# Optimization experiments

Measured on AMD Instinct MI355X. Metric: run time of the kernel, lower is better.

## Reference

```python
import jax, jax.numpy as jnp
import numpy as np
import math

D_MODEL = 1024
MEM_SIZE = 4096
N_HEADS = 8
BATCH = 4
SEQ = 1024
TOP_K = min(SEQ, MEM_SIZE // 10)  # 409, matches torch: min(seq_len, memory_size//10)
UPDATE_RATE = 0.01


def _gelu(x):
    return jax.nn.gelu(x, approximate=False)  # torch nn.GELU default (erf)


def setup_inputs() -> dict:
    key = jax.random.key(0)
    ks = jax.random.split(key, 26)
    w = lambda k, shape, s=0.02: (jax.random.normal(k, shape, jnp.float32) * s)
    inp = {
        "x": jax.random.normal(ks[0], (BATCH, SEQ, D_MODEL), jnp.float32),
        "memory_bank": jax.random.normal(ks[1], (MEM_SIZE, D_MODEL), jnp.float32) * 0.1,
        "memory_indices": jax.random.randint(ks[2], (BATCH, TOP_K), 0, MEM_SIZE, jnp.int32),
        # memory_encoder: Linear -> GELU -> Linear
        "enc_w1": w(ks[3], (D_MODEL, D_MODEL)), "enc_b1": jnp.zeros((D_MODEL,), jnp.float32),
        "enc_w2": w(ks[4], (D_MODEL, D_MODEL)), "enc_b2": jnp.zeros((D_MODEL,), jnp.float32),
        # MultiheadAttention in/out projections
        "wq": w(ks[5], (D_MODEL, D_MODEL)), "bq": jnp.zeros((D_MODEL,), jnp.float32),
        "wk": w(ks[6], (D_MODEL, D_MODEL)), "bk": jnp.zeros((D_MODEL,), jnp.float32),
        "wv": w(ks[7], (D_MODEL, D_MODEL)), "bv": jnp.zeros((D_MODEL,), jnp.float32),
        "wo": w(ks[8], (D_MODEL, D_MODEL)), "bo": jnp.zeros((D_MODEL,), jnp.float32),
        # memory_decoder: Linear -> GELU -> Linear
        "dec_w1": w(ks[9], (D_MODEL, D_MODEL)), "dec_b1": jnp.zeros((D_MODEL,), jnp.float32),
        "dec_w2": w(ks[10], (D_MODEL, D_MODEL)), "dec_b2": jnp.zeros((D_MODEL,), jnp.float32),
        # LayerNorm
        "ln_g": jnp.ones((D_MODEL,), jnp.float32), "ln_b": jnp.zeros((D_MODEL,), jnp.float32),
        # importance_scorer: Linear(d,64) -> GELU -> Linear(64,1) -> Sigmoid
        "imp_w1": w(ks[11], (D_MODEL, 64)), "imp_b1": jnp.zeros((64,), jnp.float32),
        "imp_w2": w(ks[12], (64, 1)), "imp_b2": jnp.zeros((1,), jnp.float32),
    }
    return inp


def reference(x, memory_bank, memory_indices,
              enc_w1, enc_b1, enc_w2, enc_b2,
              wq, bq, wk, bk, wv, bv, wo, bo,
              dec_w1, dec_b1, dec_w2, dec_b2,
              ln_g, ln_b, imp_w1, imp_b1, imp_w2, imp_b2):
    B, L, D = x.shape
    M = memory_bank.shape[0]
    H = N_HEADS
    dh = D // H

    # memory_encoder (dropout inactive at eval)
    enc = _gelu(x @ enc_w1 + enc_b1) @ enc_w2 + enc_b2  # [B,L,D]

    # cross-attention: query = encoded input, key/value = memory bank (shared across batch)
    q = (enc @ wq + bq).reshape(B, L, H, dh)
    k = (memory_bank @ wk + bk).reshape(M, H, dh)
    v = (memory_bank @ wv + bv).reshape(M, H, dh)
    scores = jnp.einsum('blhd,mhd->bhlm', q, k) * (1.0 / math.sqrt(dh))
    attn = jax.nn.softmax(scores, axis=-1)                 # [B,H,L,M]
    ctx = jnp.einsum('bhlm,mhd->blhd', attn, v).reshape(B, L, D)
    mem_out = ctx @ wo + bo

    # memory_decoder + residual + LayerNorm
    dec = _gelu(mem_out @ dec_w1 + dec_b1) @ dec_w2 + dec_b2
    comb = x + dec
    mu = jnp.mean(comb, axis=-1, keepdims=True)
    var = jnp.var(comb, axis=-1, keepdims=True)
    out = (comb - mu) / jnp.sqrt(var + 1e-5) * ln_g + ln_b  # [B,L,D]

    # _update_memory: importance top-k select + sequential EMA scatter into memory bank
    imp = jax.nn.sigmoid(_gelu(x @ imp_w1 + imp_b1) @ imp_w2 + imp_b2)[..., 0]  # [B,L]
    _, top_idx = jax.lax.top_k(imp, TOP_K)                  # [B,K]
    top_tok = jnp.take_along_axis(x, top_idx[..., None], axis=1)  # [B,K,D]

    # faithful to the torch double loop (b outer, k inner): sequential EMA with
    # chained updates on index collisions
    flat_idx = memory_indices.reshape(-1)
    flat_tok = top_tok.reshape(-1, D)

    def body(mem, xs):
        i, t = xs
        row = (1.0 - UPDATE_RATE) * mem[i] + UPDATE_RATE * t
        return mem.at[i].set(row), None

    new_mem, _ = jax.lax.scan(body, memory_bank, (flat_idx, flat_tok))
    return out, new_mem
```

## Files before the change

### kernel.cpp

```cpp
#include <hip/hip_runtime.h>

typedef unsigned short u16;
typedef __attribute__((ext_vector_type(4))) int i4;
typedef __attribute__((ext_vector_type(4))) unsigned u4;
typedef __attribute__((ext_vector_type(4))) unsigned short us4;
typedef __attribute__((ext_vector_type(8))) short short8;
typedef __attribute__((ext_vector_type(4))) float f4;

#define D_MODEL 1024
#define ROWS 4096
#define NHEAD 8
#define DH 128
#define TOPK 409
#define NUPD 1636
#define NBATCH 4
#define MAXC 64
#define ATTNROWS 32768

__device__ __forceinline__ u16 f2bf(float f) {
  unsigned u = __builtin_bit_cast(unsigned, f);
  u += 0x7fffu + ((u >> 16) & 1u);
  return (u16)(u >> 16);
}
__device__ __forceinline__ float bf2f(u16 b) {
  unsigned u = ((unsigned)b) << 16;
  return __builtin_bit_cast(float, u);
}
__device__ __forceinline__ float gelu_f(float v) {
  return 0.5f * v * (1.0f + erff(v * 0.70710678118654752f));
}
__device__ __forceinline__ void gload16(const void* g, void* l) {
  __builtin_amdgcn_global_load_lds((const __attribute__((address_space(1))) void*)g,
                                   (__attribute__((address_space(3))) void*)l, 16, 0, 0);
}

__global__ __launch_bounds__(256) void conv_kernel(const float* __restrict__ in,
                                                   u16* __restrict__ out, int n4) {
  int i = blockIdx.x * 256 + threadIdx.x;
  if (i < n4) {
    f4 v = ((const f4*)in)[i];
    us4 o;
    o.x = f2bf(v.x); o.y = f2bf(v.y); o.z = f2bf(v.z); o.w = f2bf(v.w);
    ((us4*)out)[i] = o;
  }
}

__global__ __launch_bounds__(256) void wtrans8_kernel(const float* s0, const float* s1,
                                                      const float* s2, const float* s3,
                                                      const float* s4, const float* s5,
                                                      const float* s6, const float* s7,
                                                      u16* __restrict__ dst) {
  const float* srcs[8] = {s0, s1, s2, s3, s4, s5, s6, s7};
  const float* w = srcs[blockIdx.z];
  u16* wt = dst + (size_t)blockIdx.z * (1024 * 1024);
  __shared__ float t[32][33];
  int tx = threadIdx.x & 31, ty = threadIdx.x >> 5;
  int k0 = blockIdx.y * 32, n0 = blockIdx.x * 32;
  for (int r = 0; r < 4; ++r)
    t[ty + r * 8][tx] = w[(size_t)(k0 + ty + r * 8) * 1024 + n0 + tx];
  __syncthreads();
  for (int r = 0; r < 4; ++r)
    wt[(size_t)(n0 + ty + r * 8) * 1024 + k0 + tx] = f2bf(t[tx][ty + r * 8]);
}

template <int EPI>
__global__ __launch_bounds__(256) void gemm_bt(const u16* __restrict__ A,
                                               const u16* __restrict__ BT,
                                               const float* __restrict__ bias,
                                               void* __restrict__ C) {
  __shared__ __align__(16) char al[2 * 128 * 64];
  __shared__ __align__(16) char bl[2 * 64 * 64];
  const int K = 1024, N = 1024;
  const int id = blockIdx.x;
  const int xcd = id & 7, j = id >> 3;
  const int m0 = ((j & 3) * 8 + xcd) * 128;
  const int n0 = (j >> 2) * 64;
  const int tid = threadIdx.x;
  const int lane = tid & 63, wid = tid >> 6;
  const int g = lane >> 4, qi = lane & 15;
  const int wr = wid >> 1, wc = wid & 1;
  f4 acc[4][2] = {};

  const int a0r = tid >> 2, a0b = (tid & 3) ^ ((a0r >> 1) & 3);
  const int c1 = tid + 256;
  const int a1r = c1 >> 2, a1b = (c1 & 3) ^ ((a1r >> 1) & 3);
  const int b0r = tid >> 2, b0b = (tid & 3) ^ ((b0r >> 1) & 3);

#define STAGE(buf, kt)                                                                   \
  {                                                                                      \
    const int k0_ = (kt) * 32;                                                           \
    gload16(A + (size_t)(m0 + a0r) * K + k0_ + a0b * 8, al + (buf) * 8192 + tid * 16);   \
    gload16(A + (size_t)(m0 + a1r) * K + k0_ + a1b * 8, al + (buf) * 8192 + c1 * 16);    \
    gload16(BT + (size_t)(n0 + b0r) * K + k0_ + b0b * 8, bl + (buf) * 4096 + tid * 16);  \
  }

  STAGE(0, 0);
  __syncthreads();
  int cur = 0;
  for (int kt = 0; kt < 32; ++kt) {
    if (kt + 1 < 32) STAGE(cur ^ 1, kt + 1);
    short8 af[4], bfr[2];
    for (int i = 0; i < 4; ++i) {
      int r = wr * 64 + i * 16 + qi;
      af[i] = *(const short8*)(al + cur * 8192 + r * 64 + ((g ^ ((r >> 1) & 3))) * 16);
    }
    for (int sn = 0; sn < 2; ++sn) {
      int r = wc * 32 + sn * 16 + qi;
      bfr[sn] = *(const short8*)(bl + cur * 4096 + r * 64 + ((g ^ ((r >> 1) & 3))) * 16);
    }
    for (int i = 0; i < 4; ++i)
      for (int sn = 0; sn < 2; ++sn)
        acc[i][sn] = __builtin_amdgcn_mfma_f32_16x16x32_bf16(af[i], bfr[sn], acc[i][sn], 0, 0, 0);
    __syncthreads();
    cur ^= 1;
  }
#undef STAGE

  for (int i = 0; i < 4; ++i) {
    int row = m0 + wr * 64 + i * 16 + g * 4;
    for (int sn = 0; sn < 2; ++sn) {
      int col = n0 + wc * 32 + sn * 16 + qi;
      float bv = bias[col];
      for (int jj = 0; jj < 4; ++jj) {
        float v = acc[i][sn][jj] + bv;
        if constexpr (EPI == 1) v = gelu_f(v);
        if constexpr (EPI == 2)
          ((float*)C)[(size_t)(row + jj) * N + col] = v;
        else
          ((u16*)C)[(size_t)(row + jj) * N + col] = f2bf(v);
      }
    }
  }
}

__global__ __launch_bounds__(256) void gemm_kv(const u16* __restrict__ A,
                                               const u16* __restrict__ BT,
                                               const float* __restrict__ bk,
                                               const float* __restrict__ bv,
                                               u16* __restrict__ Ck, u16* __restrict__ CvT) {
  __shared__ __align__(16) char pool[2 * 128 * 64 + 2 * 64 * 64];
  char* al = pool;
  char* bl = pool + 2 * 128 * 64;
  const int id = blockIdx.x;
  const int xcd = id & 7, j = id >> 3;
  const int m0 = ((j & 3) * 8 + xcd) * 128;
  const int n0 = (j >> 2) * 64;
  const int tid = threadIdx.x;
  const int lane = tid & 63, wid = tid >> 6;
  const int g = lane >> 4, qi = lane & 15;
  const int wr = wid >> 1, wc = wid & 1;
  const int K = 1024, M = 4096;
  f4 acc[4][2] = {};

  const int a0r = tid >> 2, a0b = (tid & 3) ^ ((a0r >> 1) & 3);
  const int c1 = tid + 256;
  const int a1r = c1 >> 2, a1b = (c1 & 3) ^ ((a1r >> 1) & 3);
  const int b0r = tid >> 2, b0b = (tid & 3) ^ ((b0r >> 1) & 3);

#define STAGE(buf, kt)                                                                   \
  {                                                                                      \
    const int k0_ = (kt) * 32;                                                           \
    gload16(A + (size_t)(m0 + a0r) * K + k0_ + a0b * 8, al + (buf) * 8192 + tid * 16);   \
    gload16(A + (size_t)(m0 + a1r) * K + k0_ + a1b * 8, al + (buf) * 8192 + c1 * 16);    \
    gload16(BT + (size_t)(n0 + b0r) * K + k0_ + b0b * 8, bl + (buf) * 4096 + tid * 16);  \
  }

  STAGE(0, 0);
  __syncthreads();
  int cur = 0;
  for (int kt = 0; kt < 32; ++kt) {
    if (kt + 1 < 32) STAGE(cur ^ 1, kt + 1);
    short8 af[4], bfr[2];
    for (int i = 0; i < 4; ++i) {
      int r = wr * 64 + i * 16 + qi;
      af[i] = *(const short8*)(al + cur * 8192 + r * 64 + ((g ^ ((r >> 1) & 3))) * 16);
    }
    for (int sn = 0; sn < 2; ++sn) {
      int r = wc * 32 + sn * 16 + qi;
      bfr[sn] = *(const short8*)(bl + cur * 4096 + r * 64 + ((g ^ ((r >> 1) & 3))) * 16);
    }
    for (int i = 0; i < 4; ++i)
      for (int sn = 0; sn < 2; ++sn)
        acc[i][sn] = __builtin_amdgcn_mfma_f32_16x16x32_bf16(af[i], bfr[sn], acc[i][sn], 0, 0, 0);
    __syncthreads();
    cur ^= 1;
  }
#undef STAGE

  if (n0 < 1024) {
    for (int i = 0; i < 4; ++i) {
      int row = m0 + wr * 64 + i * 16 + g * 4;
      for (int sn = 0; sn < 2; ++sn) {
        int col = n0 + wc * 32 + sn * 16 + qi;
        float bvv = bk[col];
        for (int jj = 0; jj < 4; ++jj)
          Ck[(size_t)(row + jj) * 1024 + col] = f2bf(acc[i][sn][jj] + bvv);
      }
    }
  } else {
    u16(*t)[132] = (u16(*)[132])pool;
    __syncthreads();
    for (int i = 0; i < 4; ++i)
      for (int sn = 0; sn < 2; ++sn) {
        int nl = wc * 32 + sn * 16 + qi;
        float bvv = bv[n0 - 1024 + nl];
        for (int jj = 0; jj < 4; ++jj)
          t[nl][wr * 64 + i * 16 + g * 4 + jj] = f2bf(acc[i][sn][jj] + bvv);
      }
    __syncthreads();
    int r = tid >> 2, cg = tid & 3;
    for (int v = 0; v < 4; ++v) {
      us4 val = *(const us4*)&t[r][cg * 32 + v * 8];
      *(us4*)&CvT[(size_t)(n0 - 1024 + r) * M + m0 + cg * 32 + v * 8] = val;
    }
  }
}

template <int LP>
__global__ __launch_bounds__(512) void attn_kernel(const u16* __restrict__ q,
                                                   const u16* __restrict__ kp,
                                                   const u16* __restrict__ vT,
                                                   u16* __restrict__ cp0, u16* __restrict__ cp1,
                                                   u16* __restrict__ cp2, u16* __restrict__ cp3,
                                                   float* __restrict__ ml) {
  constexpr int MR = 4096 >> LP;
  constexpr int NT = MR / 64;
  __shared__ __align__(16) char kl[64 * 256];
  __shared__ __align__(16) char vl[128 * 128];
  const int id = blockIdx.x;
  const int h = id & 7;
  const int rest = id >> 3;
  const int part = rest & ((1 << LP) - 1);
  const int qblk = (rest >> LP) & 7;
  const int b = rest >> (3 + LP);
  const int tid = threadIdx.x;
  const int lane = tid & 63, wid = tid >> 6;
  const int g = lane >> 4, qi = lane & 15;
  const int qrow = b * 1024 + qblk * 128 + wid * 16 + qi;
  const float scale = 0.08838834764831845f;
  u16* ctp = (part == 0) ? cp0 : (part == 1) ? cp1 : (part == 2) ? cp2 : cp3;

  short8 qf[4];
  for (int kk = 0; kk < 4; ++kk)
    qf[kk] = *(const short8*)(q + (size_t)qrow * 1024 + h * 128 + kk * 32 + g * 8);

  const int kc0 = tid, kc1 = tid + 512;
  const int kr0 = kc0 >> 4, kb0 = kc0 & 15, kr1 = kc1 >> 4, kb1 = kc1 & 15;
  const int vr0 = kc0 >> 3, vb0 = kc0 & 7, vr1 = kc1 >> 3, vb1 = kc1 & 7;
  const int kd0 = kr0 * 256 + (kb0 ^ (kr0 & 7)) * 16;
  const int kd1 = kr1 * 256 + (kb1 ^ (kr1 & 7)) * 16;
  const int vd0 = vr0 * 128 + (vb0 ^ (vr0 & 7)) * 16;
  const int vd1 = vr1 * 128 + (vb1 ^ (vr1 & 7)) * 16;
  const int mbase = part * MR;
  const u16* kg0 = kp + (size_t)kr0 * 1024 + h * 128 + kb0 * 8;
  const u16* kg1 = kp + (size_t)kr1 * 1024 + h * 128 + kb1 * 8;
  const u16* vg0 = vT + (size_t)(h * 128 + vr0) * 4096 + vb0 * 8;
  const u16* vg1 = vT + (size_t)(h * 128 + vr1) * 4096 + vb1 * 8;

  i4 kreg0, kreg1, vreg0, vreg1;
#define LOADREGS(mt_)                                  \
  {                                                    \
    const int m0_ = mbase + (mt_) * 64;                \
    kreg0 = *(const i4*)(kg0 + (size_t)m0_ * 1024);    \
    kreg1 = *(const i4*)(kg1 + (size_t)m0_ * 1024);    \
    vreg0 = *(const i4*)(vg0 + m0_);                   \
    vreg1 = *(const i4*)(vg1 + m0_);                   \
  }

  f4 ct[8] = {};
  float mrun = -1e30f, lsum = 0.0f;

  LOADREGS(0);
  for (int mt = 0; mt < NT; ++mt) {
    __syncthreads();
    *(i4*)(kl + kd0) = kreg0;
    *(i4*)(kl + kd1) = kreg1;
    *(i4*)(vl + vd0) = vreg0;
    *(i4*)(vl + vd1) = vreg1;
    __syncthreads();
    if (mt + 1 < NT) LOADREGS(mt + 1);

    f4 st[4] = {};
    for (int s = 0; s < 4; ++s) {
      int n = s * 16 + qi;
      const char* krow = kl + n * 256;
      int sw = n & 7;
      for (int kk = 0; kk < 4; ++kk) {
        short8 a = *(const short8*)(krow + ((kk * 4 + g) ^ sw) * 16);
        st[s] = __builtin_amdgcn_mfma_f32_16x16x32_bf16(a, qf[kk], st[s], 0, 0, 0);
      }
    }
    float sv[16];
    float tmax = -1e30f;
    for (int s = 0; s < 4; ++s)
      for (int jj = 0; jj < 4; ++jj) {
        float v = st[s][jj] * scale;
        sv[s * 4 + jj] = v;
        tmax = fmaxf(tmax, v);
      }
    tmax = fmaxf(tmax, __shfl_xor(tmax, 16, 64));
    tmax = fmaxf(tmax, __shfl_xor(tmax, 32, 64));
    float mnew = fmaxf(mrun, tmax);
    float r = __expf(mrun - mnew);
    float psum = 0.0f;
    for (int i = 0; i < 16; ++i) {
      sv[i] = __expf(sv[i] - mnew);
      psum += sv[i];
    }
    psum += __shfl_xor(psum, 16, 64);
    psum += __shfl_xor(psum, 32, 64);
    lsum = lsum * r + psum;
    mrun = mnew;
    for (int i = 0; i < 8; ++i) ct[i] = ct[i] * r;

    unsigned pk0[4], pk1[4];
    for (int s = 0; s < 4; ++s) {
      pk0[s] = (unsigned)f2bf(sv[s * 4 + 0]) | ((unsigned)f2bf(sv[s * 4 + 1]) << 16);
      pk1[s] = (unsigned)f2bf(sv[s * 4 + 2]) | ((unsigned)f2bf(sv[s * 4 + 3]) << 16);
    }
    const int src1 = qi + ((g & 1) << 5);
    const int src2 = src1 + 16;
    const bool hi = (g & 2) != 0;
    for (int p = 0; p < 2; ++p) {
      unsigned a0 = __shfl(pk0[2 * p], src1, 64), b0 = __shfl(pk0[2 * p + 1], src1, 64);
      unsigned a1 = __shfl(pk1[2 * p], src1, 64), b1 = __shfl(pk1[2 * p + 1], src1, 64);
      unsigned a2 = __shfl(pk0[2 * p], src2, 64), b2 = __shfl(pk0[2 * p + 1], src2, 64);
      unsigned a3 = __shfl(pk1[2 * p], src2, 64), b3 = __shfl(pk1[2 * p + 1], src2, 64);
      u4 bw;
      bw.x = hi ? b0 : a0; bw.y = hi ? b1 : a1; bw.z = hi ? b2 : a2; bw.w = hi ? b3 : a3;
      short8 pf = __builtin_bit_cast(short8, bw);
      for (int d = 0; d < 8; ++d) {
        int dr = d * 16 + qi;
        short8 a = *(const short8*)(vl + dr * 128 + (((p * 4 + g) ^ (dr & 7))) * 16);
        ct[d] = __builtin_amdgcn_mfma_f32_16x16x32_bf16(a, pf, ct[d], 0, 0, 0);
      }
    }
  }
#undef LOADREGS

  const int orow = ((b * 8 + h) << 10) + qblk * 128 + wid * 16 + qi;
  if (g == 0) {
    ml[(size_t)(part * ATTNROWS + orow) * 2 + 0] = mrun;
    ml[(size_t)(part * ATTNROWS + orow) * 2 + 1] = lsum;
  }
  for (int d = 0; d < 8; ++d) {
    us4 o;
    o.x = f2bf(ct[d][0]); o.y = f2bf(ct[d][1]);
    o.z = f2bf(ct[d][2]); o.w = f2bf(ct[d][3]);
    *(us4*)(ctp + (size_t)orow * 128 + d * 16 + g * 4) = o;
  }
}

__global__ __launch_bounds__(256) void combine4_kernel(const u16* __restrict__ cp0,
                                                       const u16* __restrict__ cp1,
                                                       const u16* __restrict__ cp2,
                                                       const u16* __restrict__ cp3,
                                                       const float* __restrict__ ml,
                                                       u16* __restrict__ ctx) {
  int tid = threadIdx.x;
  int row = blockIdx.x * 16 + (tid >> 4);
  int dp = (tid & 15) * 8;
  float m0 = ml[(size_t)row * 2], l0 = ml[(size_t)row * 2 + 1];
  float m1 = ml[((size_t)ATTNROWS + row) * 2], l1 = ml[((size_t)ATTNROWS + row) * 2 + 1];
  float m2 = ml[((size_t)2 * ATTNROWS + row) * 2], l2 = ml[((size_t)2 * ATTNROWS + row) * 2 + 1];
  float m3 = ml[((size_t)3 * ATTNROWS + row) * 2], l3 = ml[((size_t)3 * ATTNROWS + row) * 2 + 1];
  float m = fmaxf(fmaxf(m0, m1), fmaxf(m2, m3));
  float s0 = __expf(m0 - m), s1 = __expf(m1 - m), s2 = __expf(m2 - m), s3 = __expf(m3 - m);
  float inv = 1.0f / (l0 * s0 + l1 * s1 + l2 * s2 + l3 * s3);
  short8 c0 = *(const short8*)(cp0 + (size_t)row * 128 + dp);
  short8 c1 = *(const short8*)(cp1 + (size_t)row * 128 + dp);
  short8 c2 = *(const short8*)(cp2 + (size_t)row * 128 + dp);
  short8 c3 = *(const short8*)(cp3 + (size_t)row * 128 + dp);
  us4 o[2];
  for (int i = 0; i < 8; ++i) {
    float f = (bf2f((u16)c0[i]) * s0 + bf2f((u16)c1[i]) * s1 + bf2f((u16)c2[i]) * s2 +
               bf2f((u16)c3[i]) * s3) * inv;
    ((u16*)o)[i] = f2bf(f);
  }
  int bb = row >> 13, hh = (row >> 10) & 7, qr = row & 1023;
  *(short8*)(ctx + (size_t)((bb << 10) + qr) * 1024 + hh * 128 + dp) =
      __builtin_bit_cast(short8, o);
}

__global__ __launch_bounds__(256) void ln_kernel(const float* __restrict__ x,
                                                 const float* __restrict__ dec,
                                                 const float* __restrict__ gw,
                                                 const float* __restrict__ bw,
                                                 float* __restrict__ out,
                                                 int* __restrict__ cnt) {
  __shared__ float rs[256], rs2[256];
  int row = blockIdx.x, tid = threadIdx.x;
  if (tid == 0) cnt[row] = 0;
  float c[4];
  float s = 0.0f, s2 = 0.0f;
  for (int i = 0; i < 4; ++i) {
    int col = tid + i * 256;
    float v = x[(size_t)row * 1024 + col] + dec[(size_t)row * 1024 + col];
    c[i] = v; s += v; s2 += v * v;
  }
  rs[tid] = s; rs2[tid] = s2;
  __syncthreads();
  for (int st = 128; st > 0; st >>= 1) {
    if (tid < st) { rs[tid] += rs[tid + st]; rs2[tid] += rs2[tid + st]; }
    __syncthreads();
  }
  float mu = rs[0] * (1.0f / 1024.0f);
  float var = rs2[0] * (1.0f / 1024.0f) - mu * mu;
  float inv = rsqrtf(var + 1e-5f);
  for (int i = 0; i < 4; ++i) {
    int col = tid + i * 256;
    out[(size_t)row * 1024 + col] = (c[i] - mu) * inv * gw[col] + bw[col];
  }
}

__global__ __launch_bounds__(256) void imp_kernel(const float* __restrict__ x,
                                                  const float* __restrict__ w1,
                                                  const float* __restrict__ b1,
                                                  const float* __restrict__ w2,
                                                  const float* __restrict__ b2,
                                                  float* __restrict__ imp) {
  __shared__ float xs[8][1024];
  int tid = threadIdx.x;
  int lane = tid & 63, wid = tid >> 6;
  size_t base = (size_t)blockIdx.x * 8192;
  for (int i = 0; i < 32; ++i) ((float*)xs)[tid + i * 256] = x[base + tid + i * 256];
  __syncthreads();
  int r0 = wid * 2, r1 = wid * 2 + 1;
  float a0 = 0.0f, a1 = 0.0f;
  for (int k = 0; k < 1024; ++k) {
    float wv = w1[k * 64 + lane];
    a0 += xs[r0][k] * wv;
    a1 += xs[r1][k] * wv;
  }
  float h0 = gelu_f(a0 + b1[lane]) * w2[lane];
  float h1 = gelu_f(a1 + b1[lane]) * w2[lane];
  for (int d = 1; d < 64; d <<= 1) {
    h0 += __shfl_xor(h0, d, 64);
    h1 += __shfl_xor(h1, d, 64);
  }
  if (lane == 0) {
    imp[blockIdx.x * 8 + r0] = 1.0f / (1.0f + expf(-(h0 + b2[0])));
    imp[blockIdx.x * 8 + r1] = 1.0f / (1.0f + expf(-(h1 + b2[0])));
  }
}

__global__ __launch_bounds__(512) void topk_kernel(const float* __restrict__ imp,
                                                   int* __restrict__ tidx) {
  __shared__ float v[1024];
  __shared__ int ix[1024];
  int b = blockIdx.x, tid = threadIdx.x;
  for (int i = tid; i < 1024; i += 512) { v[i] = imp[b * 1024 + i]; ix[i] = i; }
  __syncthreads();
  for (int k = 2; k <= 1024; k <<= 1) {
    for (int j = k >> 1; j > 0; j >>= 1) {
      for (int t = tid; t < 1024; t += 512) {
        int p = t ^ j;
        if (p > t) {
          float va = v[t], vb = v[p];
          int ia = ix[t], ib = ix[p];
          bool ord = (va > vb) || (va == vb && ia < ib);
          bool up = ((t & k) == 0);
          if (up ? !ord : ord) { v[t] = vb; v[p] = va; ix[t] = ib; ix[p] = ia; }
        }
      }
      __syncthreads();
    }
  }
  for (int t = tid; t < TOPK; t += 512) tidx[b * TOPK + t] = ix[t];
}

__global__ __launch_bounds__(128) void rank_kernel(const int* __restrict__ midx,
                                                   int* __restrict__ cnt,
                                                   int* __restrict__ slot) {
  __shared__ int mi[NUPD];
  int tid = threadIdx.x;
  for (int i = tid; i < NUPD; i += 128) mi[i] = midx[i];
  __syncthreads();
  int j = blockIdx.x * 128 + tid;
  if (j < NUPD) {
    int r = mi[j], rank = 0;
    for (int jp = 0; jp < j; ++jp) rank += (mi[jp] == r) ? 1 : 0;
    if (rank < MAXC) slot[r * MAXC + rank] = j;
    atomicAdd(&cnt[r], 1);
  }
}

__global__ __launch_bounds__(256) void apply_kernel(const float* __restrict__ x,
                                                    const float* __restrict__ mem,
                                                    const int* __restrict__ tidx,
                                                    const int* __restrict__ cnt,
                                                    const int* __restrict__ slot,
                                                    float* __restrict__ outm) {
  int row = blockIdx.x, tid = threadIdx.x;
  f4 acc = ((const f4*)(mem + (size_t)row * 1024))[tid];
  int c = cnt[row];
  c = c < MAXC ? c : MAXC;
  for (int t = 0; t < c; ++t) {
    int j = slot[row * MAXC + t];
    int b = j / TOPK;
    int tr = tidx[j];
    f4 xv = ((const f4*)(x + ((size_t)b * 1024 + tr) * 1024))[tid];
    acc = acc * 0.99f + xv * 0.01f;
  }
  ((f4*)(outm + (size_t)row * 1024))[tid] = acc;
}

extern "C" void kernel_launch(void* const* d_in, const int* in_sizes, int n_in,
                              void* d_out, int out_size, void* d_ws, size_t ws_size,
                              hipStream_t stream) {
  const float* x = (const float*)d_in[0];
  const float* memory_bank = (const float*)d_in[1];
  const int* memory_indices = (const int*)d_in[2];
  const float* enc_w1 = (const float*)d_in[3];
  const float* enc_b1 = (const float*)d_in[4];
  const float* enc_w2 = (const float*)d_in[5];
  const float* enc_b2 = (const float*)d_in[6];
  const float* wq = (const float*)d_in[7];
  const float* bq = (const float*)d_in[8];
  const float* wk = (const float*)d_in[9];
  const float* bk = (const float*)d_in[10];
  const float* wv = (const float*)d_in[11];
  const float* bv = (const float*)d_in[12];
  const float* wo = (const float*)d_in[13];
  const float* bo = (const float*)d_in[14];
  const float* dec_w1 = (const float*)d_in[15];
  const float* dec_b1 = (const float*)d_in[16];
  const float* dec_w2 = (const float*)d_in[17];
  const float* dec_b2 = (const float*)d_in[18];
  const float* ln_g = (const float*)d_in[19];
  const float* ln_b = (const float*)d_in[20];
  const float* imp_w1 = (const float*)d_in[21];
  const float* imp_b1 = (const float*)d_in[22];
  const float* imp_w2 = (const float*)d_in[23];
  const float* imp_b2 = (const float*)d_in[24];

  char* ws = (char*)d_ws;
  u16* buf0 = (u16*)(ws);
  u16* buf1 = (u16*)(ws + (8ull << 20));
  u16* buf2 = (u16*)(ws + (16ull << 20));
  u16* buf3 = (u16*)(ws + (24ull << 20));
  u16* buf4 = (u16*)(ws + (32ull << 20));
  float* decb = (float*)(ws + (40ull << 20));
  u16* wtb = (u16*)(ws + (56ull << 20));
  float* impb = (float*)(ws + (72ull << 20));
  int* tidx = (int*)(ws + (72ull << 20) + (1 << 16));
  int* cnt = (int*)buf3;
  int* slot = (int*)(ws + (24ull << 20) + (1 << 16));
  u16* cp0 = buf0;
  u16* cp1 = buf2;
  u16* cp2 = (u16*)(ws + (40ull << 20));
  u16* cp3 = (u16*)(ws + (48ull << 20));
  float* ml = (float*)(ws + (56ull << 20));

  const int NM = 1024 * 1024;
  u16* wt_e1 = wtb + 0 * NM;
  u16* wt_e2 = wtb + 1 * NM;
  u16* wt_q = wtb + 2 * NM;
  u16* wt_k = wtb + 3 * NM;
  u16* wt_o = wtb + 5 * NM;
  u16* wt_d1 = wtb + 6 * NM;
  u16* wt_d2 = wtb + 7 * NM;

  conv_kernel<<<4096, 256, 0, stream>>>(x, buf0, ROWS * D_MODEL / 4);
  conv_kernel<<<4096, 256, 0, stream>>>(memory_bank, buf2, ROWS * D_MODEL / 4);
  wtrans8_kernel<<<dim3(32, 32, 8), 256, 0, stream>>>(enc_w1, enc_w2, wq, wk, wv, wo,
                                                      dec_w1, dec_w2, wtb);

  gemm_bt<1><<<512, 256, 0, stream>>>(buf0, wt_e1, enc_b1, buf1);
  gemm_bt<0><<<512, 256, 0, stream>>>(buf1, wt_e2, enc_b2, buf0);
  gemm_bt<0><<<512, 256, 0, stream>>>(buf0, wt_q, bq, buf1);
  gemm_kv<<<1024, 256, 0, stream>>>(buf2, wt_k, bk, bv, buf3, buf4);

  attn_kernel<2><<<1024, 512, 0, stream>>>(buf1, buf3, buf4, cp0, cp1, cp2, cp3, ml);
  combine4_kernel<<<2048, 256, 0, stream>>>(cp0, cp1, cp2, cp3, ml, buf1);

  gemm_bt<0><<<512, 256, 0, stream>>>(buf1, wt_o, bo, buf0);
  gemm_bt<1><<<512, 256, 0, stream>>>(buf0, wt_d1, dec_b1, buf2);
  gemm_bt<2><<<512, 256, 0, stream>>>(buf2, wt_d2, dec_b2, decb);
  ln_kernel<<<4096, 256, 0, stream>>>(x, decb, ln_g, ln_b, (float*)d_out, cnt);

  imp_kernel<<<512, 256, 0, stream>>>(x, imp_w1, imp_b1, imp_w2, imp_b2, impb);
  topk_kernel<<<NBATCH, 512, 0, stream>>>(impb, tidx);
  rank_kernel<<<13, 128, 0, stream>>>(memory_indices, cnt, slot);
  apply_kernel<<<4096, 256, 0, stream>>>(x, memory_bank, tidx, cnt, slot,
                                         (float*)d_out + (size_t)ROWS * D_MODEL);
}
```

Measured before the change: 442.2 us.

## Fold back-to-back linear layers into precomputed weight products and merge GEMM launches

Enc_w2 and wq are multiplied into one combined weight, and likewise wo and dec_w1, because no nonlinearity sits between them. The weight-product GEMMs and their folded biases run inside one mega kernel together with the KV projection and the first encoder GEMM. This removes two full activation GEMMs and several launches from the critical path, and the two input conversions become a single launch. The cost is extra weight-weight GEMMs on every call and rounding of the combined weights to bf16, which may change numerical error.

```diff
diff --git a/kernel.cpp b/kernel.cpp
--- a/kernel.cpp
+++ b/kernel.cpp
@@ -34,15 +34,18 @@
                                    (__attribute__((address_space(3))) void*)l, 16, 0, 0);
 }
 
-__global__ __launch_bounds__(256) void conv_kernel(const float* __restrict__ in,
-                                                   u16* __restrict__ out, int n4) {
-  int i = blockIdx.x * 256 + threadIdx.x;
-  if (i < n4) {
-    f4 v = ((const f4*)in)[i];
-    us4 o;
-    o.x = f2bf(v.x); o.y = f2bf(v.y); o.z = f2bf(v.z); o.w = f2bf(v.w);
-    ((us4*)out)[i] = o;
-  }
+__global__ __launch_bounds__(256) void conv2_kernel(const float* __restrict__ in0,
+                                                    u16* __restrict__ out0,
+                                                    const float* __restrict__ in1,
+                                                    u16* __restrict__ out1, int nb) {
+  int bid = blockIdx.x;
+  const float* in = (bid < nb) ? in0 : in1;
+  u16* out = (bid < nb) ? out0 : out1;
+  int i = (bid < nb ? bid : bid - nb) * 256 + threadIdx.x;
+  f4 v = ((const f4*)in)[i];
+  us4 o;
+  o.x = f2bf(v.x); o.y = f2bf(v.y); o.z = f2bf(v.z); o.w = f2bf(v.w);
+  ((us4*)out)[i] = o;
 }
 
 __global__ __launch_bounds__(256) void wtrans8_kernel(const float* s0, const float* s1,
@@ -63,6 +66,166 @@
     wt[(size_t)(n0 + ty + r * 8) * 1024 + k0 + tx] = f2bf(t[tx][ty + r * 8]);
 }
 
+__global__ __launch_bounds__(256) void bias_partB(const float* __restrict__ pbuf,
+                                                  const float* __restrict__ bq,
+                                                  const float* __restrict__ db1,
+                                                  float* __restrict__ bqp,
+                                                  float* __restrict__ bodp) {
+  int id = blockIdx.x;
+  int which = id >> 2;
+  int n = (id & 3) * 256 + threadIdx.x;
+  float s = 0.0f;
+  for (int kb = 0; kb < 8; ++kb) s += pbuf[(size_t)(which * 8 + kb) * 1024 + n];
+  float* out = which ? bodp : bqp;
+  const float* badd = which ? db1 : bq;
+  out[n] = s + badd[n];
+}
+
+__device__ __forceinline__ void gemm_core(const u16* __restrict__ A,
+                                          const u16* __restrict__ BT,
+                                          char* al, char* bl, int m0, int n0,
+                                          f4 acc[4][2]) {
+  const int K = 1024;
+  const int tid = threadIdx.x;
+  const int lane = tid & 63;
+  const int g = lane >> 4, qi = lane & 15;
+  const int wid = tid >> 6;
+  const int wr = wid >> 1, wc = wid & 1;
+  const int a0r = tid >> 2, a0b = (tid & 3) ^ ((a0r >> 1) & 3);
+  const int c1 = tid + 256;
+  const int a1r = c1 >> 2, a1b = (c1 & 3) ^ ((a1r >> 1) & 3);
+  const int b0r = tid >> 2, b0b = (tid & 3) ^ ((b0r >> 1) & 3);
+
+#define STAGE(buf, kt)                                                                   \
+  {                                                                                      \
+    const int k0_ = (kt) * 32;                                                           \
+    gload16(A + (size_t)(m0 + a0r) * K + k0_ + a0b * 8, al + (buf) * 8192 + tid * 16);   \
+    gload16(A + (size_t)(m0 + a1r) * K + k0_ + a1b * 8, al + (buf) * 8192 + c1 * 16);    \
+    gload16(BT + (size_t)(n0 + b0r) * K + k0_ + b0b * 8, bl + (buf) * 4096 + tid * 16);  \
+  }
+
+  STAGE(0, 0);
+  __syncthreads();
+  int cur = 0;
+  for (int kt = 0; kt < 32; ++kt) {
+    if (kt + 1 < 32) STAGE(cur ^ 1, kt + 1);
+    short8 af[4], bfr[2];
+    for (int i = 0; i < 4; ++i) {
+      int r = wr * 64 + i * 16 + qi;
+      af[i] = *(const short8*)(al + cur * 8192 + r * 64 + ((g ^ ((r >> 1) & 3))) * 16);
+    }
+    for (int sn = 0; sn < 2; ++sn) {
+      int r = wc * 32 + sn * 16 + qi;
+      bfr[sn] = *(const short8*)(bl + cur * 4096 + r * 64 + ((g ^ ((r >> 1) & 3))) * 16);
+    }
+    for (int i = 0; i < 4; ++i)
+      for (int sn = 0; sn < 2; ++sn)
+        acc[i][sn] = __builtin_amdgcn_mfma_f32_16x16x32_bf16(af[i], bfr[sn], acc[i][sn], 0, 0, 0);
+    __syncthreads();
+    cur ^= 1;
+  }
+#undef STAGE
+}
+
+__global__ __launch_bounds__(256) void mega_kernel(
+    const u16* __restrict__ Akv, const u16* __restrict__ BTkv,
+    const float* __restrict__ bk, const float* __restrict__ bv,
+    u16* __restrict__ Ck, u16* __restrict__ CvT,
+    const u16* __restrict__ Ae, const u16* __restrict__ BTe,
+    const float* __restrict__ be, u16* __restrict__ Ce,
+    const u16* __restrict__ A0, const u16* __restrict__ B0, u16* __restrict__ C0,
+    const u16* __restrict__ A1, const u16* __restrict__ B1, u16* __restrict__ C1,
+    const float* __restrict__ b2, const float* __restrict__ wqf,
+    const float* __restrict__ bo, const float* __restrict__ dw1,
+    float* __restrict__ pbuf) {
+  __shared__ __align__(16) char pool[2 * 128 * 64 + 2 * 64 * 64];
+  char* al = pool;
+  char* bl = pool + 2 * 128 * 64;
+  const int gid = blockIdx.x;
+  const int tid = threadIdx.x;
+  const int lane = tid & 63, wid = tid >> 6;
+  const int g = lane >> 4, qi = lane & 15;
+  const int wr = wid >> 1, wc = wid & 1;
+
+  if (gid < 1024) {
+    const int xcd = gid & 7, j = gid >> 3;
+    const int m0 = ((j & 3) * 8 + xcd) * 128;
+    const int n0 = (j >> 2) * 64;
+    f4 acc[4][2] = {};
+    gemm_core(Akv, BTkv, al, bl, m0, n0, acc);
+    if (n0 < 1024) {
+      for (int i = 0; i < 4; ++i) {
+        int row = m0 + wr * 64 + i * 16 + g * 4;
+        for (int sn = 0; sn < 2; ++sn) {
+          int col = n0 + wc * 32 + sn * 16 + qi;
+          float bvv = bk[col];
+          for (int jj = 0; jj < 4; ++jj)
+            Ck[(size_t)(row + jj) * 1024 + col] = f2bf(acc[i][sn][jj] + bvv);
+        }
+      }
+    } else {
+      u16(*t)[132] = (u16(*)[132])pool;
+      __syncthreads();
+      for (int i = 0; i < 4; ++i)
+        for (int sn = 0; sn < 2; ++sn) {
+          int nl = wc * 32 + sn * 16 + qi;
+          float bvv = bv[n0 - 1024 + nl];
+          for (int jj = 0; jj < 4; ++jj)
+            t[nl][wr * 64 + i * 16 + g * 4 + jj] = f2bf(acc[i][sn][jj] + bvv);
+        }
+      __syncthreads();
+      int r = tid >> 2, cg = tid & 3;
+      for (int v = 0; v < 4; ++v) {
+        us4 val = *(const us4*)&t[r][cg * 32 + v * 8];
+        *(us4*)&CvT[(size_t)(n0 - 1024 + r) * 4096 + m0 + cg * 32 + v * 8] = val;
+      }
+    }
+  } else if (gid < 1536) {
+    const int id = gid - 1024;
+    const int xcd = id & 7, j = id >> 3;
+    const int m0 = ((j & 3) * 8 + xcd) * 128;
+    const int n0 = (j >> 2) * 64;
+    f4 acc[4][2] = {};
+    gemm_core(Ae, BTe, al, bl, m0, n0, acc);
+    for (int i = 0; i < 4; ++i) {
+      int row = m0 + wr * 64 + i * 16 + g * 4;
+      for (int sn = 0; sn < 2; ++sn) {
+        int col = n0 + wc * 32 + sn * 16 + qi;
+        float bv = be[col];
+        for (int jj = 0; jj < 4; ++jj)
+          Ce[(size_t)(row + jj) * 1024 + col] = f2bf(gelu_f(acc[i][sn][jj] + bv));
+      }
+    }
+  } else if (gid < 1792) {
+    const int id = gid - 1536;
+    const int which = id >> 7, j = id & 127;
+    const u16* A = which ? A1 : A0;
+    const u16* BT = which ? B1 : B0;
+    u16* C = which ? C1 : C0;
+    const int m0 = (j >> 4) * 128, n0 = (j & 15) * 64;
+    f4 acc[4][2] = {};
+    gemm_core(A, BT, al, bl, m0, n0, acc);
+    for (int i = 0; i < 4; ++i) {
+      int row = m0 + wr * 64 + i * 16 + g * 4;
+      for (int sn = 0; sn < 2; ++sn) {
+        int col = n0 + wc * 32 + sn * 16 + qi;
+        for (int jj = 0; jj < 4; ++jj)
+          C[(size_t)(row + jj) * 1024 + col] = f2bf(acc[i][sn][jj]);
+      }
+    }
+  } else {
+    const int lid = gid - 1792;
+    const int which = lid >> 5;
+    const int kb = (lid >> 2) & 7;
+    const int n = (lid & 3) * 256 + tid;
+    const float* bvec = which ? bo : b2;
+    const float* W = which ? dw1 : wqf;
+    float s = 0.0f;
+    for (int k = kb * 128; k < kb * 128 + 128; ++k) s += bvec[k] * W[(size_t)k * 1024 + n];
+    pbuf[(size_t)(which * 8 + kb) * 1024 + n] = s;
+  }
+}
+
 template <int EPI>
 __global__ __launch_bounds__(256) void gemm_bt(const u16* __restrict__ A,
                                                const u16* __restrict__ BT,
@@ -70,7 +233,7 @@
                                                void* __restrict__ C) {
   __shared__ __align__(16) char al[2 * 128 * 64];
   __shared__ __align__(16) char bl[2 * 64 * 64];
-  const int K = 1024, N = 1024;
+  const int N = 1024;
   const int id = blockIdx.x;
   const int xcd = id & 7, j = id >> 3;
   const int m0 = ((j & 3) * 8 + xcd) * 128;
@@ -80,42 +243,7 @@
   const int g = lane >> 4, qi = lane & 15;
   const int wr = wid >> 1, wc = wid & 1;
   f4 acc[4][2] = {};
-
-  const int a0r = tid >> 2, a0b = (tid & 3) ^ ((a0r >> 1) & 3);
-  const int c1 = tid + 256;
-  const int a1r = c1 >> 2, a1b = (c1 & 3) ^ ((a1r >> 1) & 3);
-  const int b0r = tid >> 2, b0b = (tid & 3) ^ ((b0r >> 1) & 3);
-
-#define STAGE(buf, kt)                                                                   \
-  {                                                                                      \
-    const int k0_ = (kt) * 32;                                                           \
-    gload16(A + (size_t)(m0 + a0r) * K + k0_ + a0b * 8, al + (buf) * 8192 + tid * 16);   \
-    gload16(A + (size_t)(m0 + a1r) * K + k0_ + a1b * 8, al + (buf) * 8192 + c1 * 16);    \
-    gload16(BT + (size_t)(n0 + b0r) * K + k0_ + b0b * 8, bl + (buf) * 4096 + tid * 16);  \
-  }
-
-  STAGE(0, 0);
-  __syncthreads();
-  int cur = 0;
-  for (int kt = 0; kt < 32; ++kt) {
-    if (kt + 1 < 32) STAGE(cur ^ 1, kt + 1);
-    short8 af[4], bfr[2];
-    for (int i = 0; i < 4; ++i) {
-      int r = wr * 64 + i * 16 + qi;
-      af[i] = *(const short8*)(al + cur * 8192 + r * 64 + ((g ^ ((r >> 1) & 3))) * 16);
-    }
-    for (int sn = 0; sn < 2; ++sn) {
-      int r = wc * 32 + sn * 16 + qi;
-      bfr[sn] = *(const short8*)(bl + cur * 4096 + r * 64 + ((g ^ ((r >> 1) & 3))) * 16);
-    }
-    for (int i = 0; i < 4; ++i)
-      for (int sn = 0; sn < 2; ++sn)
-        acc[i][sn] = __builtin_amdgcn_mfma_f32_16x16x32_bf16(af[i], bfr[sn], acc[i][sn], 0, 0, 0);
-    __syncthreads();
-    cur ^= 1;
-  }
-#undef STAGE
-
+  gemm_core(A, BT, al, bl, m0, n0, acc);
   for (int i = 0; i < 4; ++i) {
     int row = m0 + wr * 64 + i * 16 + g * 4;
     for (int sn = 0; sn < 2; ++sn) {
@@ -129,89 +257,6 @@
         else
           ((u16*)C)[(size_t)(row + jj) * N + col] = f2bf(v);
       }
-    }
-  }
-}
-
-__global__ __launch_bounds__(256) void gemm_kv(const u16* __restrict__ A,
-                                               const u16* __restrict__ BT,
-                                               const float* __restrict__ bk,
-                                               const float* __restrict__ bv,
-                                               u16* __restrict__ Ck, u16* __restrict__ CvT) {
-  __shared__ __align__(16) char pool[2 * 128 * 64 + 2 * 64 * 64];
-  char* al = pool;
-  char* bl = pool + 2 * 128 * 64;
-  const int id = blockIdx.x;
-  const int xcd = id & 7, j = id >> 3;
-  const int m0 = ((j & 3) * 8 + xcd) * 128;
-  const int n0 = (j >> 2) * 64;
-  const int tid = threadIdx.x;
-  const int lane = tid & 63, wid = tid >> 6;
-  const int g = lane >> 4, qi = lane & 15;
-  const int wr = wid >> 1, wc = wid & 1;
-  const int K = 1024, M = 4096;
-  f4 acc[4][2] = {};
-
-  const int a0r = tid >> 2, a0b = (tid & 3) ^ ((a0r >> 1) & 3);
-  const int c1 = tid + 256;
-  const int a1r = c1 >> 2, a1b = (c1 & 3) ^ ((a1r >> 1) & 3);
-  const int b0r = tid >> 2, b0b = (tid & 3) ^ ((b0r >> 1) & 3);
-
-#define STAGE(buf, kt)                                                                   \
-  {                                                                                      \
-    const int k0_ = (kt) * 32;                                                           \
-    gload16(A + (size_t)(m0 + a0r) * K + k0_ + a0b * 8, al + (buf) * 8192 + tid * 16);   \
-    gload16(A + (size_t)(m0 + a1r) * K + k0_ + a1b * 8, al + (buf) * 8192 + c1 * 16);    \
-    gload16(BT + (size_t)(n0 + b0r) * K + k0_ + b0b * 8, bl + (buf) * 4096 + tid * 16);  \
-  }
-
-  STAGE(0, 0);
-  __syncthreads();
-  int cur = 0;
-  for (int kt = 0; kt < 32; ++kt) {
-    if (kt + 1 < 32) STAGE(cur ^ 1, kt + 1);
-    short8 af[4], bfr[2];
-    for (int i = 0; i < 4; ++i) {
-      int r = wr * 64 + i * 16 + qi;
-      af[i] = *(const short8*)(al + cur * 8192 + r * 64 + ((g ^ ((r >> 1) & 3))) * 16);
-    }
-    for (int sn = 0; sn < 2; ++sn) {
-      int r = wc * 32 + sn * 16 + qi;
-      bfr[sn] = *(const short8*)(bl + cur * 4096 + r * 64 + ((g ^ ((r >> 1) & 3))) * 16);
-    }
-    for (int i = 0; i < 4; ++i)
-      for (int sn = 0; sn < 2; ++sn)
-        acc[i][sn] = __builtin_amdgcn_mfma_f32_16x16x32_bf16(af[i], bfr[sn], acc[i][sn], 0, 0, 0);
-    __syncthreads();
-    cur ^= 1;
-  }
-#undef STAGE
-
-  if (n0 < 1024) {
-    for (int i = 0; i < 4; ++i) {
-      int row = m0 + wr * 64 + i * 16 + g * 4;
-      for (int sn = 0; sn < 2; ++sn) {
-        int col = n0 + wc * 32 + sn * 16 + qi;
-        float bvv = bk[col];
-        for (int jj = 0; jj < 4; ++jj)
-          Ck[(size_t)(row + jj) * 1024 + col] = f2bf(acc[i][sn][jj] + bvv);
-      }
-    }
-  } else {
-    u16(*t)[132] = (u16(*)[132])pool;
-    __syncthreads();
-    for (int i = 0; i < 4; ++i)
-      for (int sn = 0; sn < 2; ++sn) {
-        int nl = wc * 32 + sn * 16 + qi;
-        float bvv = bv[n0 - 1024 + nl];
-        for (int jj = 0; jj < 4; ++jj)
-          t[nl][wr * 64 + i * 16 + g * 4 + jj] = f2bf(acc[i][sn][jj] + bvv);
-      }
-    __syncthreads();
-    int r = tid >> 2, cg = tid & 3;
-    for (int v = 0; v < 4; ++v) {
-      us4 val = *(const us4*)&t[r][cg * 32 + v * 8];
-      *(us4*)&CvT[(size_t)(n0 - 1024 + r) * M + m0 + cg * 32 + v * 8] = val;
     }
   }
 }
@@ -544,9 +589,14 @@
   u16* wtb = (u16*)(ws + (56ull << 20));
   float* impb = (float*)(ws + (72ull << 20));
   int* tidx = (int*)(ws + (72ull << 20) + (1 << 16));
+  float* bqp = (float*)(ws + (72ull << 20) + (1 << 17));
+  float* bodp = (float*)(ws + (72ull << 20) + (1 << 17) + 4096);
+  float* pbuf = (float*)(ws + (72ull << 20) + 196608);
   int* cnt = (int*)buf3;
   int* slot = (int*)(ws + (24ull << 20) + (1 << 16));
-  u16* cp0 = buf0;
+  u16* w2n = (u16*)(ws + (40ull << 20));
+  u16* won = (u16*)(ws + (42ull << 20));
+  u16* cp0 = buf1;
   u16* cp1 = buf2;
   u16* cp2 = (u16*)(ws + (40ull << 20));
   u16* cp3 = (u16*)(ws + (48ull << 20));
@@ -554,29 +604,31 @@
 
   const int NM = 1024 * 1024;
   u16* wt_e1 = wtb + 0 * NM;
-  u16* wt_e2 = wtb + 1 * NM;
+  u16* wt_e2q = wtb + 1 * NM;
   u16* wt_q = wtb + 2 * NM;
   u16* wt_k = wtb + 3 * NM;
-  u16* wt_o = wtb + 5 * NM;
+  u16* wt_od = wtb + 5 * NM;
   u16* wt_d1 = wtb + 6 * NM;
   u16* wt_d2 = wtb + 7 * NM;
 
-  conv_kernel<<<4096, 256, 0, stream>>>(x, buf0, ROWS * D_MODEL / 4);
-  conv_kernel<<<4096, 256, 0, stream>>>(memory_bank, buf2, ROWS * D_MODEL / 4);
+  conv2_kernel<<<8192, 256, 0, stream>>>(x, buf0, memory_bank, buf2, 4096);
   wtrans8_kernel<<<dim3(32, 32, 8), 256, 0, stream>>>(enc_w1, enc_w2, wq, wk, wv, wo,
                                                       dec_w1, dec_w2, wtb);
-
-  gemm_bt<1><<<512, 256, 0, stream>>>(buf0, wt_e1, enc_b1, buf1);
-  gemm_bt<0><<<512, 256, 0, stream>>>(buf1, wt_e2, enc_b2, buf0);
-  gemm_bt<0><<<512, 256, 0, stream>>>(buf0, wt_q, bq, buf1);
-  gemm_kv<<<1024, 256, 0, stream>>>(buf2, wt_k, bk, bv, buf3, buf4);
-
-  attn_kernel<2><<<1024, 512, 0, stream>>>(buf1, buf3, buf4, cp0, cp1, cp2, cp3, ml);
-  combine4_kernel<<<2048, 256, 0, stream>>>(cp0, cp1, cp2, cp3, ml, buf1);
-
-  gemm_bt<0><<<512, 256, 0, stream>>>(buf1, wt_o, bo, buf0);
-  gemm_bt<1><<<512, 256, 0, stream>>>(buf0, wt_d1, dec_b1, buf2);
-  gemm_bt<2><<<512, 256, 0, stream>>>(buf2, wt_d2, dec_b2, decb);
+  conv2_kernel<<<2048, 256, 0, stream>>>(enc_w2, w2n, wo, won, 1024);
+
+  mega_kernel<<<1856, 256, 0, stream>>>(buf2, wt_k, bk, bv, buf3, buf4,
+                                        buf0, wt_e1, enc_b1, buf1,
+                                        wt_q, w2n, wt_e2q, wt_d1, won, wt_od,
+                                        enc_b2, wq, bo, dec_w1, pbuf);
+  bias_partB<<<8, 256, 0, stream>>>(pbuf, bq, dec_b1, bqp, bodp);
+
+  gemm_bt<0><<<512, 256, 0, stream>>>(buf1, wt_e2q, bqp, buf0);
+
+  attn_kernel<2><<<1024, 512, 0, stream>>>(buf0, buf3, buf4, cp0, cp1, cp2, cp3, ml);
+  combine4_kernel<<<2048, 256, 0, stream>>>(cp0, cp1, cp2, cp3, ml, buf0);
+
+  gemm_bt<1><<<512, 256, 0, stream>>>(buf0, wt_od, bodp, buf1);
+  gemm_bt<2><<<512, 256, 0, stream>>>(buf1, wt_d2, dec_b2, decb);
   ln_kernel<<<4096, 256, 0, stream>>>(x, decb, ln_g, ln_b, (float*)d_out, cnt);
 
   imp_kernel<<<512, 256, 0, stream>>>(x, imp_w1, imp_b1, imp_w2, imp_b2, impb);
```

After: 398.8 us. -9.8%, faster.
